# Kernel tuning notes

Hardware: AMD Instinct MI355X
Metric: run time of the kernel (lower is better)

## Reference

```python
import jax, jax.numpy as jnp
import numpy as np

HIDDEN = 4096
SPARSITY_RATIO = 0.1
BLOCK_SIZE = max(1, int(HIDDEN * SPARSITY_RATIO * 2))  # 819, matches torch block_diagonal


def _block_diag_mask(h: int, block_size: int) -> jnp.ndarray:
    # mask[i, j] = True iff i and j fall in the same diagonal block of size block_size
    # (last block may be partial) -- equivalent to the torch loop via floor division
    idx = jnp.arange(h) // block_size
    return idx[:, None] == idx[None, :]


def setup_inputs() -> dict:
    key = jax.random.key(0)
    kx, kw = jax.random.split(key)
    x = jax.random.normal(kx, (8, 2048, HIDDEN), dtype=jnp.float32)
    mask = _block_diag_mask(HIDDEN, BLOCK_SIZE)
    eye = jnp.eye(HIDDEN, dtype=jnp.float32)
    W = eye + 0.1 * jax.random.normal(kw, (HIDDEN, HIDDEN), dtype=jnp.float32)
    # replicate torch init: masked noise on-pattern, identity off-pattern
    W = W * mask.astype(jnp.float32) + eye * (~mask).astype(jnp.float32)
    return {"x": x, "W": W, "mask": mask}


def reference(x, W, mask):
    sparse_W = W * mask.astype(W.dtype)           # [H, H]
    return jnp.einsum('bsh,oh->bso', x, sparse_W)  # x @ sparse_W.T
```

## Files before the change

kernel.cpp:

```cpp
#include <hip/hip_runtime.h>
#include <hip/hip_bf16.h>

#define H       4096
#define BS      819
#define NB      5
#define KPAD    832
#define NPAD    896
#define M_TOTAL 16384
#define XB_LD   (NB * KPAD)

typedef __bf16 bf16x8 __attribute__((ext_vector_type(8)));
typedef float  f32x4  __attribute__((ext_vector_type(4)));

__device__ __forceinline__ void gld_lds16(const void* gptr, void* ldsptr) {
    __builtin_amdgcn_global_load_lds(
        (const __attribute__((address_space(1))) void*)gptr,
        (__attribute__((address_space(3))) void*)ldsptr,
        16, 0, 0);
}

__global__ void pack_x_kernel(const float* __restrict__ x,
                              __hip_bfloat16* __restrict__ xb) {
    const int m  = blockIdx.y;
    const int j4 = (blockIdx.x * blockDim.x + threadIdx.x) * 4;
    if (j4 >= XB_LD) return;
    const int g  = j4 / KPAD;
    const int jj = j4 - g * KPAD;
    const float* xr = x + (size_t)m * H + g * BS;
    union { __hip_bfloat16 h[4]; uint2 u; } v;
#pragma unroll
    for (int i = 0; i < 4; ++i) {
        float f = (jj + i < BS) ? xr[jj + i] : 0.f;
        v.h[i] = __float2bfloat16(f);
    }
    *reinterpret_cast<uint2*>(xb + (size_t)m * XB_LD + j4) = v.u;
}

__global__ void pack_w_kernel(const float* __restrict__ W,
                              __hip_bfloat16* __restrict__ wb) {
    const int g   = blockIdx.y;
    const int idx = blockIdx.x * blockDim.x + threadIdx.x;
    if (idx >= NPAD * KPAD) return;
    const int n = idx / KPAD;
    const int k = idx - n * KPAD;
    float v = 0.f;
    if (n < BS && k < BS)
        v = W[(size_t)(g * BS + n) * H + g * BS + k];
    wb[(size_t)g * NPAD * KPAD + idx] = __float2bfloat16(v);
}

__global__ void last_col_kernel(const float* __restrict__ x,
                                const float* __restrict__ W,
                                float* __restrict__ out) {
    const int m = blockIdx.x * blockDim.x + threadIdx.x;
    if (m >= M_TOTAL) return;
    const float w = W[(size_t)4095 * H + 4095];
    out[(size_t)m * H + 4095] = x[(size_t)m * H + 4095] * w;
}

__global__ void gemm_kernel(const __hip_bfloat16* __restrict__ xb,
                            const __hip_bfloat16* __restrict__ wb,
                            float* __restrict__ out) {
    __shared__ __hip_bfloat16 lA[128 * 32];
    __shared__ __hip_bfloat16 lB[128 * 32];

    const int tid   = threadIdx.x;
    const int mBase = blockIdx.x * 128;
    const int nBase = blockIdx.y * 128;
    const int g     = blockIdx.z;
    const int lane  = tid & 63;
    const int wave  = tid >> 6;
    const int waveM = wave >> 1;
    const int waveN = wave & 1;
    const int quad  = lane >> 4;
    const int l16   = lane & 15;

    const int c0 = tid,        r0 = c0 >> 2, kq0 = (c0 & 3) * 8;
    const int c1 = tid + 256,  r1 = c1 >> 2, kq1 = (c1 & 3) * 8;

    const __hip_bfloat16* a0 = xb + (size_t)(mBase + r0) * XB_LD + (size_t)g * KPAD + kq0;
    const __hip_bfloat16* a1 = xb + (size_t)(mBase + r1) * XB_LD + (size_t)g * KPAD + kq1;
    const __hip_bfloat16* b0 = wb + ((size_t)g * NPAD + nBase + r0) * KPAD + kq0;
    const __hip_bfloat16* b1 = wb + ((size_t)g * NPAD + nBase + r1) * KPAD + kq1;

    char* lAb = (char*)lA;
    char* lBb = (char*)lB;

    f32x4 acc[4][4] = {};

    for (int kt = 0; kt < KPAD / 32; ++kt) {
        const int k0 = kt * 32;
        gld_lds16(a0 + k0, lAb + c0 * 16);
        gld_lds16(a1 + k0, lAb + c1 * 16);
        gld_lds16(b0 + k0, lBb + c0 * 16);
        gld_lds16(b1 + k0, lBb + c1 * 16);
        __syncthreads();

        bf16x8 a[4], b[4];
#pragma unroll
        for (int mi = 0; mi < 4; ++mi)
            a[mi] = *reinterpret_cast<const bf16x8*>(lA + (waveM * 64 + mi * 16 + l16) * 32 + quad * 8);
#pragma unroll
        for (int ni = 0; ni < 4; ++ni)
            b[ni] = *reinterpret_cast<const bf16x8*>(lB + (waveN * 64 + ni * 16 + l16) * 32 + quad * 8);

#pragma unroll
        for (int mi = 0; mi < 4; ++mi)
#pragma unroll
            for (int ni = 0; ni < 4; ++ni)
                acc[mi][ni] = __builtin_amdgcn_mfma_f32_16x16x32_bf16(a[mi], b[ni], acc[mi][ni], 0, 0, 0);
        __syncthreads();
    }

#pragma unroll
    for (int mi = 0; mi < 4; ++mi) {
        const int mrow = mBase + waveM * 64 + mi * 16 + quad * 4;
#pragma unroll
        for (int ni = 0; ni < 4; ++ni) {
            const int ncol = nBase + waveN * 64 + ni * 16 + l16;
            if (ncol < BS) {
                float* op = out + (size_t)mrow * H + (size_t)g * BS + ncol;
#pragma unroll
                for (int r = 0; r < 4; ++r)
                    op[(size_t)r * H] = acc[mi][ni][r];
            }
        }
    }
}

__global__ void fallback_kernel(const float* __restrict__ x,
                                const float* __restrict__ W,
                                float* __restrict__ out) {
    const size_t idx = (size_t)blockIdx.x * blockDim.x + threadIdx.x;
    if (idx >= (size_t)M_TOTAL * H) return;
    const int m = (int)(idx / H);
    const int o = (int)(idx % H);
    const int g = o / BS;
    const int h0 = g * BS;
    const int len = (g < NB) ? BS : 1;
    const float* xr = x + (size_t)m * H + h0;
    const float* wr = W + (size_t)o * H + h0;
    float s = 0.f;
    for (int k = 0; k < len; ++k) s += xr[k] * wr[k];
    out[idx] = s;
}

extern "C" void kernel_launch(void* const* d_in, const int* in_sizes, int n_in,
                              void* d_out, int out_size, void* d_ws, size_t ws_size,
                              hipStream_t stream) {
    const float* x = (const float*)d_in[0];
    const float* W = (const float*)d_in[1];
    float* out = (float*)d_out;

    const size_t xb_elems = (size_t)M_TOTAL * XB_LD;
    const size_t wb_elems = (size_t)NB * NPAD * KPAD;
    const size_t need = (xb_elems + wb_elems) * sizeof(__hip_bfloat16);

    if (ws_size < need) {
        const size_t total = (size_t)M_TOTAL * H;
        fallback_kernel<<<(unsigned)((total + 255) / 256), 256, 0, stream>>>(x, W, out);
        return;
    }

    __hip_bfloat16* xb = (__hip_bfloat16*)d_ws;
    __hip_bfloat16* wb = xb + xb_elems;

    pack_x_kernel<<<dim3((XB_LD / 4 + 255) / 256, M_TOTAL), 256, 0, stream>>>(x, xb);
    pack_w_kernel<<<dim3((NPAD * KPAD + 255) / 256, NB), 256, 0, stream>>>(W, wb);
    gemm_kernel<<<dim3(M_TOTAL / 128, NPAD / 128, NB), 256, 0, stream>>>(xb, wb, out);
    last_col_kernel<<<(M_TOTAL + 255) / 256, 256, 0, stream>>>(x, W, out);
}
```

Baseline: 685.5 us.

## Vectorize packing with per-group shift and pad LDS rows against bank conflicts

The x packing kernel now reads float4 from x and writes each group's data at a small per-group offset so the writes stay aligned, zeroing the padding in a separate block. The W packing kernel writes four bf16 at a time and applies the same shift so the K indices still line up. The GEMM pads each LDS row to 40 elements, spreading rows across banks, and spreads the 16-byte direct-to-LDS copies over five slots per thread, with dummy copies into the unused pad slots. The aim is to cut the cost of the memory-bound packing pass and LDS bank conflicts, at the price of more complex indexing and some extra copy instructions.

```diff
diff --git a/kernel.cpp b/kernel.cpp
--- a/kernel.cpp
+++ b/kernel.cpp
@@ -8,6 +8,10 @@
 #define NPAD    896
 #define M_TOTAL 16384
 #define XB_LD   (NB * KPAD)
+#define RS      40
+#define TILE_CH 640
+
+#define SHIFT(g) ((3 * (g)) & 3)
 
 typedef __bf16 bf16x8 __attribute__((ext_vector_type(8)));
 typedef float  f32x4  __attribute__((ext_vector_type(4)));
@@ -21,32 +25,61 @@
 
 __global__ void pack_x_kernel(const float* __restrict__ x,
                               __hip_bfloat16* __restrict__ xb) {
-    const int m  = blockIdx.y;
-    const int j4 = (blockIdx.x * blockDim.x + threadIdx.x) * 4;
-    if (j4 >= XB_LD) return;
-    const int g  = j4 / KPAD;
-    const int jj = j4 - g * KPAD;
-    const float* xr = x + (size_t)m * H + g * BS;
-    union { __hip_bfloat16 h[4]; uint2 u; } v;
-#pragma unroll
-    for (int i = 0; i < 4; ++i) {
-        float f = (jj + i < BS) ? xr[jj + i] : 0.f;
-        v.h[i] = __float2bfloat16(f);
-    }
-    *reinterpret_cast<uint2*>(xb + (size_t)m * XB_LD + j4) = v.u;
+    const int m = blockIdx.y;
+    if (blockIdx.x == 4) {
+        const int t = threadIdx.x;
+        if (t < NB * 13) {
+            const int g = t / 13, k = t % 13;
+            const int shift = SHIFT(g);
+            const int off = (k < shift) ? k : (BS + k);
+            xb[(size_t)m * XB_LD + g * KPAD + off] = __float2bfloat16(0.f);
+        }
+        return;
+    }
+    const int q  = blockIdx.x * 256 + threadIdx.x;
+    const int j0 = q * 4;
+    const float4 v = *reinterpret_cast<const float4*>(x + (size_t)m * H + j0);
+    const int g0 = j0 / BS;
+    const int g3 = (j0 + 3) / BS;
+    if (g0 == g3) {
+        const size_t o = (size_t)m * XB_LD + g0 * KPAD + SHIFT(g0) + (j0 - g0 * BS);
+        union { __hip_bfloat16 h[4]; uint2 u; } tt;
+        tt.h[0] = __float2bfloat16(v.x);
+        tt.h[1] = __float2bfloat16(v.y);
+        tt.h[2] = __float2bfloat16(v.z);
+        tt.h[3] = __float2bfloat16(v.w);
+        *reinterpret_cast<uint2*>(xb + o) = tt.u;
+    } else {
+        const float vv[4] = { v.x, v.y, v.z, v.w };
+#pragma unroll
+        for (int i = 0; i < 4; ++i) {
+            const int j = j0 + i;
+            if (j >= NB * BS) continue;
+            const int g = j / BS;
+            xb[(size_t)m * XB_LD + g * KPAD + SHIFT(g) + (j - g * BS)] =
+                __float2bfloat16(vv[i]);
+        }
+    }
 }
 
 __global__ void pack_w_kernel(const float* __restrict__ W,
                               __hip_bfloat16* __restrict__ wb) {
-    const int g   = blockIdx.y;
-    const int idx = blockIdx.x * blockDim.x + threadIdx.x;
-    if (idx >= NPAD * KPAD) return;
-    const int n = idx / KPAD;
-    const int k = idx - n * KPAD;
-    float v = 0.f;
-    if (n < BS && k < BS)
-        v = W[(size_t)(g * BS + n) * H + g * BS + k];
-    wb[(size_t)g * NPAD * KPAD + idx] = __float2bfloat16(v);
+    const int g  = blockIdx.y;
+    const int p4 = (blockIdx.x * 256 + threadIdx.x) * 4;
+    if (p4 >= NPAD * KPAD) return;
+    const int n  = p4 / KPAD;
+    const int k0 = p4 - n * KPAD;
+    const int shift = SHIFT(g);
+    union { __hip_bfloat16 h[4]; uint2 u; } tt;
+#pragma unroll
+    for (int i = 0; i < 4; ++i) {
+        const int k = k0 + i - shift;
+        float val = 0.f;
+        if (n < BS && k >= 0 && k < BS)
+            val = W[(size_t)(g * BS + n) * H + g * BS + k];
+        tt.h[i] = __float2bfloat16(val);
+    }
+    *reinterpret_cast<uint2*>(wb + (size_t)g * NPAD * KPAD + p4) = tt.u;
 }
 
 __global__ void last_col_kernel(const float* __restrict__ x,
@@ -61,8 +94,8 @@
 __global__ void gemm_kernel(const __hip_bfloat16* __restrict__ xb,
                             const __hip_bfloat16* __restrict__ wb,
                             float* __restrict__ out) {
-    __shared__ __hip_bfloat16 lA[128 * 32];
-    __shared__ __hip_bfloat16 lB[128 * 32];
+    __shared__ __hip_bfloat16 lA[128 * RS];
+    __shared__ __hip_bfloat16 lB[128 * RS];
 
     const int tid   = threadIdx.x;
     const int mBase = blockIdx.x * 128;
@@ -74,35 +107,40 @@
     const int waveN = wave & 1;
     const int quad  = lane >> 4;
     const int l16   = lane & 15;
-
-    const int c0 = tid,        r0 = c0 >> 2, kq0 = (c0 & 3) * 8;
-    const int c1 = tid + 256,  r1 = c1 >> 2, kq1 = (c1 & 3) * 8;
-
-    const __hip_bfloat16* a0 = xb + (size_t)(mBase + r0) * XB_LD + (size_t)g * KPAD + kq0;
-    const __hip_bfloat16* a1 = xb + (size_t)(mBase + r1) * XB_LD + (size_t)g * KPAD + kq1;
-    const __hip_bfloat16* b0 = wb + ((size_t)g * NPAD + nBase + r0) * KPAD + kq0;
-    const __hip_bfloat16* b1 = wb + ((size_t)g * NPAD + nBase + r1) * KPAD + kq1;
-
-    char* lAb = (char*)lA;
-    char* lBb = (char*)lB;
+    (void)lane;
+
+    const __hip_bfloat16* src[5];
+    __hip_bfloat16*       dst[5];
+#pragma unroll
+    for (int s = 0; s < 5; ++s) {
+        const int u   = tid + 256 * s;
+        const bool isA = (u < TILE_CH);
+        const int c   = isA ? u : (u - TILE_CH);
+        const int r   = c / 5;
+        const int rem = c - r * 5;
+        const int rr  = (rem < 4) ? r : 0;
+        const int kk  = (rem < 4) ? rem * 8 : 0;
+        src[s] = isA ? (xb + (size_t)(mBase + rr) * XB_LD + (size_t)g * KPAD + kk)
+                     : (wb + ((size_t)g * NPAD + nBase + rr) * KPAD + kk);
+        dst[s] = (isA ? lA : lB) + c * 8;
+    }
 
     f32x4 acc[4][4] = {};
 
     for (int kt = 0; kt < KPAD / 32; ++kt) {
         const int k0 = kt * 32;
-        gld_lds16(a0 + k0, lAb + c0 * 16);
-        gld_lds16(a1 + k0, lAb + c1 * 16);
-        gld_lds16(b0 + k0, lBb + c0 * 16);
-        gld_lds16(b1 + k0, lBb + c1 * 16);
+#pragma unroll
+        for (int s = 0; s < 5; ++s)
+            gld_lds16(src[s] + k0, dst[s]);
         __syncthreads();
 
         bf16x8 a[4], b[4];
 #pragma unroll
         for (int mi = 0; mi < 4; ++mi)
-            a[mi] = *reinterpret_cast<const bf16x8*>(lA + (waveM * 64 + mi * 16 + l16) * 32 + quad * 8);
+            a[mi] = *reinterpret_cast<const bf16x8*>(lA + (waveM * 64 + mi * 16 + l16) * RS + quad * 8);
 #pragma unroll
         for (int ni = 0; ni < 4; ++ni)
-            b[ni] = *reinterpret_cast<const bf16x8*>(lB + (waveN * 64 + ni * 16 + l16) * 32 + quad * 8);
+            b[ni] = *reinterpret_cast<const bf16x8*>(lB + (waveN * 64 + ni * 16 + l16) * RS + quad * 8);
 
 #pragma unroll
         for (int mi = 0; mi < 4; ++mi)
@@ -165,8 +203,8 @@
     __hip_bfloat16* xb = (__hip_bfloat16*)d_ws;
     __hip_bfloat16* wb = xb + xb_elems;
 
-    pack_x_kernel<<<dim3((XB_LD / 4 + 255) / 256, M_TOTAL), 256, 0, stream>>>(x, xb);
-    pack_w_kernel<<<dim3((NPAD * KPAD + 255) / 256, NB), 256, 0, stream>>>(W, wb);
+    pack_x_kernel<<<dim3(5, M_TOTAL), 256, 0, stream>>>(x, xb);
+    pack_w_kernel<<<dim3((NPAD * KPAD / 4 + 255) / 256, NB), 256, 0, stream>>>(W, wb);
     gemm_kernel<<<dim3(M_TOTAL / 128, NPAD / 128, NB), 256, 0, stream>>>(xb, wb, out);
     last_col_kernel<<<(M_TOTAL + 255) / 256, 256, 0, stream>>>(x, W, out);
 }
```

New measurement: 693.2 us. Within noise of the previous version (+1.1%).
